# Kernel optimization log

Measured on AMD Instinct MI355X. Metric: run time of the kernel, lower is better.

## Reference

```python
import jax, jax.numpy as jnp
import numpy as np
from jax import lax

NUM_HEADS = 8
EPS = 1e-12  # torch F.normalize default eps


def setup_inputs() -> dict:
    key = jax.random.key(0)
    ks = jax.random.split(key, 7)
    B, C, H, W = 4, 128, 256, 256
    d = C // 2  # per-branch channels = 64
    x = jax.random.normal(ks[0], (B, C, H, W), jnp.float32)
    w_qkv1 = jax.random.normal(ks[1], (3 * d, d), jnp.float32) * 0.05
    w_qkv2 = jax.random.normal(ks[2], (3 * d, d), jnp.float32) * 0.05
    w_dw1 = jax.random.normal(ks[3], (3 * d, 1, 3, 3), jnp.float32) * 0.05
    w_dw2 = jax.random.normal(ks[4], (3 * d, 1, 3, 3), jnp.float32) * 0.05
    w_po1 = jax.random.normal(ks[5], (d, d), jnp.float32) * 0.05
    w_po2 = jax.random.normal(ks[6], (d, d), jnp.float32) * 0.05
    t1 = jnp.ones((NUM_HEADS, 1, 1), jnp.float32)
    t2 = jnp.ones((NUM_HEADS, 1, 1), jnp.float32)
    return {"x": x, "w_qkv1": w_qkv1, "w_qkv2": w_qkv2, "w_dw1": w_dw1,
            "w_dw2": w_dw2, "w_po1": w_po1, "w_po2": w_po2, "t1": t1, "t2": t2}


def _qkv(xb, w1x1, wdw):
    # 1x1 conv (pointwise) then 3x3 depthwise conv, no bias
    y = jnp.einsum('bchw,oc->bohw', xb, w1x1)
    y = lax.conv_general_dilated(
        y, wdw, window_strides=(1, 1), padding='SAME',
        dimension_numbers=('NCHW', 'OIHW', 'NCHW'),
        feature_group_count=y.shape[1])
    return y


def _heads(t, b, h, w):
    # b (head c) h w -> b head c (h*w)
    return t.reshape(b, NUM_HEADS, -1, h * w)


def _l2norm(t):
    n = jnp.sqrt(jnp.sum(t * t, axis=-1, keepdims=True))
    return t / jnp.maximum(n, EPS)


def reference(x, w_qkv1, w_qkv2, w_dw1, w_dw2, w_po1, w_po2, t1, t2):
    b, c, h, w = x.shape
    x1, x2 = jnp.split(x, 2, axis=1)
    q1, k1, v1 = jnp.split(_qkv(x1, w_qkv1, w_dw1), 3, axis=1)
    q2, k2, v2 = jnp.split(_qkv(x2, w_qkv2, w_dw2), 3, axis=1)
    q1, k1, v1 = (_heads(t, b, h, w) for t in (q1, k1, v1))
    q2, k2, v2 = (_heads(t, b, h, w) for t in (q2, k2, v2))
    q1, k1 = _l2norm(q1), _l2norm(k1)
    q2, k2 = _l2norm(q2), _l2norm(k2)
    # channel-wise attention: [b, head, c_h, c_h]
    attn1 = jax.nn.softmax(jnp.einsum('bhcn,bhdn->bhcd', q1, k1) * t1[None], axis=-1)
    attn2 = jax.nn.softmax(jnp.einsum('bhcn,bhdn->bhcd', q2, k2) * t2[None], axis=-1)
    # cross-branch V swap
    out1 = jnp.einsum('bhcd,bhdn->bhcn', attn1, v2).reshape(b, c // 2, h, w)
    out2 = jnp.einsum('bhcd,bhdn->bhcn', attn2, v1).reshape(b, c // 2, h, w)
    out1 = jnp.einsum('bchw,oc->bohw', out1, w_po1)
    out2 = jnp.einsum('bchw,oc->bohw', out2, w_po2)
    return jnp.concatenate([out1, out2], axis=1)
```

## Files before the change

### kernel.cpp

```cpp
#include <hip/hip_runtime.h>
#include <hip/hip_fp16.h>

#define NPIX 65536
#define WIMG 256
#define HIMG 256
#define TW 16
#define TH 8
#define HSTR 24
#define NSLOT 240
#define YCH 248

typedef __attribute__((ext_vector_type(8))) _Float16 half8;
typedef __attribute__((ext_vector_type(4))) float f32x4;

__device__ __forceinline__ unsigned int h2u(__half2 h) {
  union { __half2 h; unsigned int u; } c; c.h = h; return c.u;
}
__device__ __forceinline__ __half2 u2h(unsigned int u) {
  union { unsigned int u; __half2 h; } c; c.u = u; return c.h;
}
__device__ __forceinline__ __half2 sp2(_Float16 s) {
  union { _Float16 h[2]; __half2 v; } u; u.h[0] = s; u.h[1] = s; return u.v;
}
__device__ __forceinline__ int qk_idx(int ch, int pxblk) {
  return ch * 128 + ((pxblk ^ (ch & 7)) << 3);
}
__device__ __forceinline__ void ld16_lds(const void* g, void* l) {
  __builtin_amdgcn_global_load_lds(
      (const __attribute__((address_space(1))) unsigned int*)g,
      (__attribute__((address_space(3))) unsigned int*)l, 16, 0, 0);
}

__global__ __launch_bounds__(256)
void k_prep(const float* __restrict__ wq1, const float* __restrict__ wq2,
            const float* __restrict__ wd1, const float* __restrict__ wd2,
            float* __restrict__ zbuf,
            _Float16* __restrict__ wqh, _Float16* __restrict__ wdh) {
  int i = blockIdx.x * 256 + threadIdx.x;
  if (i < 6144) {
    zbuf[i] = 0.0f;
  } else {
    int j = i - 6144;
    if (j < 24576) {
      int br = j / 12288, r = j - br * 12288;
      wqh[j] = (_Float16)((br ? wq2 : wq1)[r]);
    } else {
      int k = j - 24576;
      int br = k / 3072, r = k - br * 3072;
      int o = r >> 4, t = r & 15;
      wdh[k] = (t < 9) ? (_Float16)((br ? wd2 : wd1)[o * 9 + t]) : (_Float16)0.0f;
    }
  }
}

__global__ __launch_bounds__(256)
void k_xt(const float* __restrict__ x, __half* __restrict__ xT) {
  __shared__ _Float16 tile[64 * 257];
  const int strip = blockIdx.x;
  const int br = blockIdx.y, b = blockIdx.z;
  const int tid = threadIdx.x;
  const float* xb = x + ((size_t)b * 128 + br * 64) * NPIX + strip * 256;
  #pragma unroll 8
  for (int c = 0; c < 64; ++c)
    tile[c * 257 + tid] = (_Float16)xb[(size_t)c * NPIX + tid];
  __syncthreads();
  __half* xo = xT + ((size_t)(b * 2 + br) * NPIX + strip * 256) * 64;
  const int j = tid & 7;
  #pragma unroll
  for (int i = 0; i < 8; ++i) {
    int p = (tid >> 3) + i * 32;
    half8 h;
    #pragma unroll
    for (int k = 0; k < 8; ++k) h[k] = tile[(j * 8 + k) * 257 + p];
    *(half8*)((_Float16*)xo + p * 64 + j * 8) = h;
  }
}

__global__ __launch_bounds__(256, 4)
void k_qkv(const __half* __restrict__ xT,
           const _Float16* __restrict__ wqh, const _Float16* __restrict__ wdh,
           const float* __restrict__ zpage,
           __half* __restrict__ vbuf, float* __restrict__ gram,
           float* __restrict__ sqq, float* __restrict__ sqk)
{
  __shared__ __align__(16) _Float16 xs[256 * 64];
  __shared__ __align__(16) _Float16 ys[16 * YCH];

  const int tid = threadIdx.x;
  const int lane = tid & 63;
  const int wid = tid >> 6;
  const int tile = blockIdx.x;
  const int br = blockIdx.y;
  const int b = blockIdx.z;
  const int tx0 = (tile & 15) * TW;
  const int ty0 = (tile >> 4) * TH;

  const _Float16* wqb = wqh + br * 12288;
  const _Float16* wdb = wdh + br * 3072;
  const __half* xTimg = xT + (size_t)(b * 2 + br) * NPIX * 64;

  {
    const int j = lane & 7, pl = lane >> 3;
    for (int it = wid; it < 30; it += 4) {
      int s = it * 8;
      int slot = s + pl;
      int hy = slot / HSTR;
      int hx = slot - hy * HSTR;
      int gy = ty0 - 1 + hy, gx = tx0 - 1 + hx;
      bool valid = (hx < 18) && ((unsigned)gy < HIMG) && ((unsigned)gx < WIMG);
      const void* src = valid
        ? (const void*)((const _Float16*)xTimg + (size_t)(gy * WIMG + gx) * 64
                        + ((j ^ (slot & 7)) << 3))
        : (const void*)((const char*)zpage + lane * 16);
      ld16_lds(src, (void*)(xs + s * 64));
    }
  }
  asm volatile("s_waitcnt vmcnt(0)" ::: "memory");
  __syncthreads();

  const int col = lane & 15;
  const int qrow = lane >> 4;
  const int rel = wid * 4 + (lane >> 4);
  const int row = (lane >> 1) & 7;
  const int half = lane & 1;

  unsigned int qreg[4][4], kreg[4][4];

#define PW16(P_, G_) do {                                                     \
    const _Float16* wp_ = wqb + ((((P_) * 64 + (G_) * 16 + col) << 6) + qrow * 8); \
    half8 wf0_ = *(const half8*)(wp_);                                        \
    half8 wf1_ = *(const half8*)(wp_ + 32);                                   \
    for (int mt = wid; mt < 15; mt += 4) {                                    \
      int px = mt * 16 + col;                                                 \
      half8 af0 = *(const half8*)(xs + px * 64 + (((qrow    ) ^ (px & 7)) << 3)); \
      half8 af1 = *(const half8*)(xs + px * 64 + (((4 + qrow) ^ (px & 7)) << 3)); \
      f32x4 a0 = {0,0,0,0};                                                   \
      a0 = __builtin_amdgcn_mfma_f32_16x16x32_f16(af0, wf0_, a0, 0, 0, 0);    \
      a0 = __builtin_amdgcn_mfma_f32_16x16x32_f16(af1, wf1_, a0, 0, 0, 0);    \
      int pxd = mt * 16 + qrow * 4;                                           \
      uint2 s0_ = {h2u(__floats2half2_rn(a0[0], a0[1])),                      \
                   h2u(__floats2half2_rn(a0[2], a0[3]))};                     \
      *(uint2*)(ys + col * YCH + pxd) = s0_;                                  \
    }                                                                         \
  } while (0)

#define DW16(P_, G_) do {                                                     \
    const int o_ = (G_) * 16 + rel;                                           \
    const _Float16* wdp_ = wdb + (((P_) * 64 + o_) << 4);                     \
    half8 wv_ = *(const half8*)wdp_;                                          \
    _Float16 w8_ = wdp_[8];                                                   \
    __half2 w2_[9];                                                           \
    _Pragma("unroll")                                                         \
    for (int j = 0; j < 8; ++j) w2_[j] = sp2(wv_[j]);                         \
    w2_[8] = sp2(w8_);                                                        \
    __half2 a_[4];                                                            \
    _Pragma("unroll")                                                         \
    for (int k2 = 0; k2 < 4; ++k2) a_[k2] = u2h(0u);                          \
    _Pragma("unroll")                                                         \
    for (int ky = 0; ky < 3; ++ky) {                                          \
      const _Float16* rp_ = ys + rel * YCH + (row + ky) * HSTR + half * 8;    \
      uint2 ra_ = *(const uint2*)rp_;                                         \
      uint2 rb_ = *(const uint2*)(rp_ + 4);                                   \
      unsigned int rc_ = *(const unsigned int*)(rp_ + 8);                     \
      unsigned int W_[5] = {ra_.x, ra_.y, rb_.x, rb_.y, rc_};                 \
      _Pragma("unroll")                                                       \
      for (int k2 = 0; k2 < 4; ++k2) {                                        \
        unsigned int M_ = (W_[k2] >> 16) | (W_[k2 + 1] << 16);                \
        a_[k2] = __hfma2(w2_[ky * 3 + 0], u2h(W_[k2]), a_[k2]);               \
        a_[k2] = __hfma2(w2_[ky * 3 + 1], u2h(M_), a_[k2]);                   \
        a_[k2] = __hfma2(w2_[ky * 3 + 2], u2h(W_[k2 + 1]), a_[k2]);           \
      }                                                                       \
    }                                                                         \
    if ((P_) == 0) {                                                          \
      _Pragma("unroll")                                                       \
      for (int k2 = 0; k2 < 4; ++k2) qreg[G_][k2] = h2u(a_[k2]);              \
    } else if ((P_) == 1) {                                                   \
      _Pragma("unroll")                                                       \
      for (int k2 = 0; k2 < 4; ++k2) kreg[G_][k2] = h2u(a_[k2]);              \
    } else {                                                                  \
      __half* vrow_ = (__half*)(vbuf                                          \
          + ((size_t)((br * 4 + b) * 64 + o_)) * NPIX                         \
          + (ty0 + row) * WIMG + tx0 + half * 8);                             \
      uint4 s_ = {h2u(a_[0]), h2u(a_[1]), h2u(a_[2]), h2u(a_[3])};            \
      *(uint4*)vrow_ = s_;                                                    \
    }                                                                         \
  } while (0)

  PW16(0, 0); __syncthreads(); DW16(0, 0); __syncthreads();
  PW16(0, 1); __syncthreads(); DW16(0, 1); __syncthreads();
  PW16(0, 2); __syncthreads(); DW16(0, 2); __syncthreads();
  PW16(0, 3); __syncthreads(); DW16(0, 3); __syncthreads();
  PW16(1, 0); __syncthreads(); DW16(1, 0); __syncthreads();
  PW16(1, 1); __syncthreads(); DW16(1, 1); __syncthreads();
  PW16(1, 2); __syncthreads(); DW16(1, 2); __syncthreads();
  PW16(1, 3); __syncthreads(); DW16(1, 3); __syncthreads();
  PW16(2, 0); __syncthreads(); DW16(2, 0); __syncthreads();
  PW16(2, 1); __syncthreads(); DW16(2, 1); __syncthreads();
  PW16(2, 2); __syncthreads(); DW16(2, 2); __syncthreads();
  PW16(2, 3); __syncthreads(); DW16(2, 3);

  {
    _Float16* qsb = xs;
    _Float16* ksb = xs + 64 * 128;
    const int pb = row * 2 + half;
    #pragma unroll
    for (int g = 0; g < 4; ++g) {
      int ch = g * 16 + rel;
      uint4 q_ = {qreg[g][0], qreg[g][1], qreg[g][2], qreg[g][3]};
      uint4 k_ = {kreg[g][0], kreg[g][1], kreg[g][2], kreg[g][3]};
      *(uint4*)(qsb + qk_idx(ch, pb)) = q_;
      *(uint4*)(ksb + qk_idx(ch, pb)) = k_;
    }
  }
  __syncthreads();

  {
    const _Float16* qsb = xs;
    const _Float16* ksb = xs + 64 * 128;
    f32x4 gqk = {0,0,0,0}, gqq = {0,0,0,0}, gkk = {0,0,0,0};
    int ch = wid * 16 + col;
    #pragma unroll
    for (int kc = 0; kc < 4; ++kc) {
      int pb = kc * 4 + qrow;
      half8 aq = *(const half8*)(qsb + qk_idx(ch, pb));
      half8 bk = *(const half8*)(ksb + qk_idx(ch, pb));
      gqk = __builtin_amdgcn_mfma_f32_16x16x32_f16(aq, bk, gqk, 0, 0, 0);
      gqq = __builtin_amdgcn_mfma_f32_16x16x32_f16(aq, aq, gqq, 0, 0, 0);
      gkk = __builtin_amdgcn_mfma_f32_16x16x32_f16(bk, bk, gkk, 0, 0, 0);
    }
    const int gb_off = (br * 4 + b);
    if (((lane >> 3) & 1) == (lane >> 5)) {
      float* gb = gram + gb_off * 512;
      int kch = ch;
      int qc0 = wid * 16 + qrow * 4;
      #pragma unroll
      for (int r = 0; r < 4; ++r) {
        int qch = qc0 + r;
        atomicAdd(&gb[(qch >> 3) * 64 + (qch & 7) * 8 + (kch & 7)], gqk[r]);
      }
    }
    if ((col >> 2) == qrow) {
      atomicAdd(&sqq[gb_off * 64 + ch], gqq[lane & 3]);
      atomicAdd(&sqk[gb_off * 64 + ch], gkk[lane & 3]);
    }
  }
#undef PW16
#undef DW16
}

__global__ __launch_bounds__(64)
void k_attn(const float* __restrict__ gram, const float* __restrict__ sqq,
            const float* __restrict__ sqk,
            const float* __restrict__ wpo1, const float* __restrict__ wpo2,
            const float* __restrict__ t1, const float* __restrict__ t2,
            _Float16* __restrict__ wefft)
{
  const int br = blockIdx.x, b = blockIdx.y;
  const int t = threadIdx.x;
  __shared__ float attn[8][8][8];
  const float* gb = gram + (br * 4 + b) * 512;
  const float* sq = sqq + (br * 4 + b) * 64;
  const float* sk = sqk + (br * 4 + b) * 64;
  const float* tt = br ? t2 : t1;
  {
    int h = t >> 3, cq = t & 7;
    float ts = tt[h];
    float qn = fmaxf(sqrtf(sq[h * 8 + cq]), 1e-12f);
    float lg[8], m = -1e30f;
    #pragma unroll
    for (int d2 = 0; d2 < 8; ++d2) {
      float kn = fmaxf(sqrtf(sk[h * 8 + d2]), 1e-12f);
      lg[d2] = ts * gb[h * 64 + cq * 8 + d2] / (qn * kn);
      m = fmaxf(m, lg[d2]);
    }
    float s = 0.f;
    #pragma unroll
    for (int d2 = 0; d2 < 8; ++d2) { lg[d2] = expf(lg[d2] - m); s += lg[d2]; }
    float inv = 1.0f / s;
    #pragma unroll
    for (int d2 = 0; d2 < 8; ++d2) attn[h][cq][d2] = lg[d2] * inv;
  }
  __syncthreads();
  const float* wpo = br ? wpo2 : wpo1;
  _Float16* wt = wefft + (br * 4 + b) * 4096;
  for (int cp = 0; cp < 64; ++cp) {
    int hp = cp >> 3, ip = cp & 7;
    float acc = 0.f;
    #pragma unroll
    for (int j = 0; j < 8; ++j)
      acc += wpo[t * 64 + hp * 8 + j] * attn[hp][j][ip];
    wt[t * 64 + cp] = (_Float16)acc;
  }
}

__global__ __launch_bounds__(256)
void k_out(const __half* __restrict__ vbuf, const _Float16* __restrict__ wefft,
           float* __restrict__ out)
{
  __shared__ __align__(16) _Float16 vs[64 * 128];
  __shared__ __align__(16) _Float16 vt[128 * 64];

  const int strip = blockIdx.x;
  const int obr = blockIdx.y, b = blockIdx.z;
  const int brv = 1 - obr;
  const int tid = threadIdx.x;
  const int lane = tid & 63;
  const int wid = tid >> 6;
  const int col = lane & 15;
  const int qrow = lane >> 4;

  const __half* vb = vbuf + ((size_t)(brv * 4 + b) * 64) * NPIX + strip * 128;

  for (int i = 0; i < 4; ++i) {
    int it = wid * 4 + i;
    const void* src = (const void*)((const _Float16*)vb
        + (size_t)(it * 4 + (lane >> 4)) * NPIX + (lane & 15) * 8);
    ld16_lds(src, (void*)(vs + it * 512));
  }
  asm volatile("s_waitcnt vmcnt(0)" ::: "memory");
  __syncthreads();

  {
    int px = tid & 127, cb = tid >> 7;
    #pragma unroll
    for (int j = 0; j < 4; ++j) {
      half8 h;
      #pragma unroll
      for (int e = 0; e < 8; ++e) h[e] = vs[(cb * 32 + j * 8 + e) * 128 + px];
      int chunk = cb * 4 + j;
      *(half8*)(vt + ((px * 8 + (chunk ^ (px & 7))) << 3)) = h;
    }
  }
  __syncthreads();

  const _Float16* wt = wefft + (obr * 4 + b) * 4096;
  half8 bf[2][4];
  #pragma unroll
  for (int nt = 0; nt < 4; ++nt)
    #pragma unroll
    for (int kc = 0; kc < 2; ++kc)
      bf[kc][nt] = *(const half8*)(wt + (nt * 16 + col) * 64 + kc * 32 + qrow * 8);

  float* ob = out + ((size_t)b * 128 + obr * 64) * NPIX + strip * 128;
  #pragma unroll
  for (int mi = 0; mi < 2; ++mi) {
    int mt = wid * 2 + mi;
    int px = mt * 16 + col;
    half8 af0 = *(const half8*)(vt + ((px * 8 + ((qrow    ) ^ (px & 7))) << 3));
    half8 af1 = *(const half8*)(vt + ((px * 8 + ((4 + qrow) ^ (px & 7))) << 3));
    f32x4 acc[4] = {{0,0,0,0},{0,0,0,0},{0,0,0,0},{0,0,0,0}};
    #pragma unroll
    for (int nt = 0; nt < 4; ++nt) {
      acc[nt] = __builtin_amdgcn_mfma_f32_16x16x32_f16(af0, bf[0][nt], acc[nt], 0, 0, 0);
      acc[nt] = __builtin_amdgcn_mfma_f32_16x16x32_f16(af1, bf[1][nt], acc[nt], 0, 0, 0);
    }
    int pxd = mt * 16 + qrow * 4;
    #pragma unroll
    for (int nt = 0; nt < 4; ++nt) {
      float4 s = {acc[nt][0], acc[nt][1], acc[nt][2], acc[nt][3]};
      *(float4*)(ob + (size_t)(nt * 16 + col) * NPIX + pxd) = s;
    }
  }
}

extern "C" void kernel_launch(void* const* d_in, const int* in_sizes, int n_in,
                              void* d_out, int out_size, void* d_ws, size_t ws_size,
                              hipStream_t stream) {
  const float* x     = (const float*)d_in[0];
  const float* wqkv1 = (const float*)d_in[1];
  const float* wqkv2 = (const float*)d_in[2];
  const float* wdw1  = (const float*)d_in[3];
  const float* wdw2  = (const float*)d_in[4];
  const float* wpo1  = (const float*)d_in[5];
  const float* wpo2  = (const float*)d_in[6];
  const float* t1    = (const float*)d_in[7];
  const float* t2    = (const float*)d_in[8];

  char* ws = (char*)d_ws;
  __half* vbuf = (__half*)ws;
  float* gram  = (float*)(ws + 67108864);
  float* sqq   = gram + 4096;
  float* sqk   = sqq + 512;
  float* zpage = sqk + 512;
  _Float16* wqkvh = (_Float16*)(zpage + 1024);
  _Float16* wdwh  = wqkvh + 24576;
  _Float16* wefft = wdwh + 6144;

  __half* xT = (__half*)d_out;

  k_prep<<<dim3(144), dim3(256), 0, stream>>>(wqkv1, wqkv2, wdw1, wdw2,
                                              gram, wqkvh, wdwh);
  k_xt<<<dim3(256, 2, 4), dim3(256), 0, stream>>>(x, xT);
  k_qkv<<<dim3(512, 2, 4), dim3(256), 0, stream>>>(xT, wqkvh, wdwh,
                                                   zpage, vbuf, gram, sqq, sqk);
  k_attn<<<dim3(2, 4), dim3(64), 0, stream>>>(gram, sqq, sqk, wpo1, wpo2, t1, t2, wefft);
  k_out<<<dim3(512, 2, 4), dim3(256), 0, stream>>>(vbuf, wefft, (float*)d_out);
}
```

Before: 240.9 us.

## Process 32 channels per pointwise/depthwise phase with prefetched weights

The fused qkv kernel now handles 32 output channels per phase instead of 16. That halves the number of pointwise/depthwise phases and their barriers, and each thread's depthwise pass covers a full 16-pixel row. Weights for the next phase are loaded into registers ahead of time (double buffering), and the q/k scatter to shared memory moves inside the final phase. The ys buffer doubles and launch bounds drop to 3 blocks per SM, so occupancy may fall in exchange for fewer syncs and wider per-thread work.

```diff
diff --git a/kernel.cpp b/kernel.cpp
--- a/kernel.cpp
+++ b/kernel.cpp
@@ -76,7 +76,7 @@
   }
 }
 
-__global__ __launch_bounds__(256, 4)
+__global__ __launch_bounds__(256, 3)
 void k_qkv(const __half* __restrict__ xT,
            const _Float16* __restrict__ wqh, const _Float16* __restrict__ wdh,
            const float* __restrict__ zpage,
@@ -84,7 +84,7 @@
            float* __restrict__ sqq, float* __restrict__ sqk)
 {
   __shared__ __align__(16) _Float16 xs[256 * 64];
-  __shared__ __align__(16) _Float16 ys[16 * YCH];
+  __shared__ __align__(16) _Float16 ys[32 * YCH];
 
   const int tid = threadIdx.x;
   const int lane = tid & 63;
@@ -120,99 +120,117 @@
 
   const int col = lane & 15;
   const int qrow = lane >> 4;
-  const int rel = wid * 4 + (lane >> 4);
-  const int row = (lane >> 1) & 7;
-  const int half = lane & 1;
-
-  unsigned int qreg[4][4], kreg[4][4];
-
-#define PW16(P_, G_) do {                                                     \
-    const _Float16* wp_ = wqb + ((((P_) * 64 + (G_) * 16 + col) << 6) + qrow * 8); \
-    half8 wf0_ = *(const half8*)(wp_);                                        \
-    half8 wf1_ = *(const half8*)(wp_ + 32);                                   \
+  const int oo = tid >> 3;
+  const int row = tid & 7;
+
+  unsigned int qreg[2][8], kreg[2][8];
+
+#define LOADW(P_, H_, F00, F01, F10, F11, WV, W8) do {                        \
+    const _Float16* wp_ = wqb + ((((P_) * 64 + (H_) * 32 + col) << 6) + qrow * 8); \
+    F00 = *(const half8*)(wp_);                                               \
+    F10 = *(const half8*)(wp_ + 32);                                          \
+    F01 = *(const half8*)(wp_ + 1024);                                        \
+    F11 = *(const half8*)(wp_ + 1024 + 32);                                   \
+    const _Float16* wdp_ = wdb + ((((P_) * 64 + (H_) * 32 + oo)) << 4);       \
+    WV = *(const half8*)wdp_;                                                 \
+    W8 = wdp_[8];                                                             \
+} while (0)
+
+#define PHASE(P_, H_, F00, F01, F10, F11, WV, W8) do {                        \
     for (int mt = wid; mt < 15; mt += 4) {                                    \
       int px = mt * 16 + col;                                                 \
       half8 af0 = *(const half8*)(xs + px * 64 + (((qrow    ) ^ (px & 7)) << 3)); \
       half8 af1 = *(const half8*)(xs + px * 64 + (((4 + qrow) ^ (px & 7)) << 3)); \
-      f32x4 a0 = {0,0,0,0};                                                   \
-      a0 = __builtin_amdgcn_mfma_f32_16x16x32_f16(af0, wf0_, a0, 0, 0, 0);    \
-      a0 = __builtin_amdgcn_mfma_f32_16x16x32_f16(af1, wf1_, a0, 0, 0, 0);    \
+      f32x4 a0 = {0,0,0,0}, a1 = {0,0,0,0};                                   \
+      a0 = __builtin_amdgcn_mfma_f32_16x16x32_f16(af0, F00, a0, 0, 0, 0);     \
+      a0 = __builtin_amdgcn_mfma_f32_16x16x32_f16(af1, F10, a0, 0, 0, 0);     \
+      a1 = __builtin_amdgcn_mfma_f32_16x16x32_f16(af0, F01, a1, 0, 0, 0);     \
+      a1 = __builtin_amdgcn_mfma_f32_16x16x32_f16(af1, F11, a1, 0, 0, 0);     \
       int pxd = mt * 16 + qrow * 4;                                           \
-      uint2 s0_ = {h2u(__floats2half2_rn(a0[0], a0[1])),                      \
-                   h2u(__floats2half2_rn(a0[2], a0[3]))};                     \
-      *(uint2*)(ys + col * YCH + pxd) = s0_;                                  \
+      __half2* d0 = (__half2*)(ys + (col     ) * YCH + pxd);                  \
+      __half2* d1 = (__half2*)(ys + (col + 16) * YCH + pxd);                  \
+      d0[0] = __floats2half2_rn(a0[0], a0[1]);                                \
+      d0[1] = __floats2half2_rn(a0[2], a0[3]);                                \
+      d1[0] = __floats2half2_rn(a1[0], a1[1]);                                \
+      d1[1] = __floats2half2_rn(a1[2], a1[3]);                                \
     }                                                                         \
-  } while (0)
-
-#define DW16(P_, G_) do {                                                     \
-    const int o_ = (G_) * 16 + rel;                                           \
-    const _Float16* wdp_ = wdb + (((P_) * 64 + o_) << 4);                     \
-    half8 wv_ = *(const half8*)wdp_;                                          \
-    _Float16 w8_ = wdp_[8];                                                   \
-    __half2 w2_[9];                                                           \
-    _Pragma("unroll")                                                         \
-    for (int j = 0; j < 8; ++j) w2_[j] = sp2(wv_[j]);                         \
-    w2_[8] = sp2(w8_);                                                        \
-    __half2 a_[4];                                                            \
-    _Pragma("unroll")                                                         \
-    for (int k2 = 0; k2 < 4; ++k2) a_[k2] = u2h(0u);                          \
-    _Pragma("unroll")                                                         \
-    for (int ky = 0; ky < 3; ++ky) {                                          \
-      const _Float16* rp_ = ys + rel * YCH + (row + ky) * HSTR + half * 8;    \
-      uint2 ra_ = *(const uint2*)rp_;                                         \
-      uint2 rb_ = *(const uint2*)(rp_ + 4);                                   \
-      unsigned int rc_ = *(const unsigned int*)(rp_ + 8);                     \
-      unsigned int W_[5] = {ra_.x, ra_.y, rb_.x, rb_.y, rc_};                 \
+    __syncthreads();                                                          \
+    {                                                                         \
+      const int o_ = (H_) * 32 + oo;                                          \
+      __half2 w2_[9];                                                         \
       _Pragma("unroll")                                                       \
-      for (int k2 = 0; k2 < 4; ++k2) {                                        \
-        unsigned int M_ = (W_[k2] >> 16) | (W_[k2 + 1] << 16);                \
-        a_[k2] = __hfma2(w2_[ky * 3 + 0], u2h(W_[k2]), a_[k2]);               \
-        a_[k2] = __hfma2(w2_[ky * 3 + 1], u2h(M_), a_[k2]);                   \
-        a_[k2] = __hfma2(w2_[ky * 3 + 2], u2h(W_[k2 + 1]), a_[k2]);           \
+      for (int j = 0; j < 8; ++j) w2_[j] = sp2(WV[j]);                        \
+      w2_[8] = sp2(W8);                                                       \
+      __half2 a_[8];                                                          \
+      _Pragma("unroll")                                                       \
+      for (int k2 = 0; k2 < 8; ++k2) a_[k2] = u2h(0u);                        \
+      _Pragma("unroll")                                                       \
+      for (int ky = 0; ky < 3; ++ky) {                                        \
+        const _Float16* rp_ = ys + oo * YCH + (row + ky) * HSTR;              \
+        uint4 ra_ = *(const uint4*)rp_;                                       \
+        uint4 rb_ = *(const uint4*)(rp_ + 8);                                 \
+        unsigned int rc_ = *(const unsigned int*)(rp_ + 16);                  \
+        unsigned int A_[9] = {ra_.x, ra_.y, ra_.z, ra_.w,                     \
+                              rb_.x, rb_.y, rb_.z, rb_.w, rc_};               \
+        _Pragma("unroll")                                                     \
+        for (int k2 = 0; k2 < 8; ++k2) {                                      \
+          unsigned int M_ = (A_[k2] >> 16) | (A_[k2 + 1] << 16);              \
+          a_[k2] = __hfma2(w2_[ky * 3 + 0], u2h(A_[k2]), a_[k2]);             \
+          a_[k2] = __hfma2(w2_[ky * 3 + 1], u2h(M_), a_[k2]);                 \
+          a_[k2] = __hfma2(w2_[ky * 3 + 2], u2h(A_[k2 + 1]), a_[k2]);         \
+        }                                                                     \
+      }                                                                       \
+      if ((P_) == 0) {                                                        \
+        _Pragma("unroll")                                                     \
+        for (int k2 = 0; k2 < 8; ++k2) qreg[H_][k2] = h2u(a_[k2]);            \
+      } else if ((P_) == 1) {                                                 \
+        _Pragma("unroll")                                                     \
+        for (int k2 = 0; k2 < 8; ++k2) kreg[H_][k2] = h2u(a_[k2]);            \
+      } else {                                                                \
+        __half* vrow_ = (__half*)(vbuf                                        \
+            + ((size_t)((br * 4 + b) * 64 + o_)) * NPIX                       \
+            + (ty0 + row) * WIMG + tx0);                                      \
+        uint4 s0_ = {h2u(a_[0]), h2u(a_[1]), h2u(a_[2]), h2u(a_[3])};         \
+        uint4 s1_ = {h2u(a_[4]), h2u(a_[5]), h2u(a_[6]), h2u(a_[7])};         \
+        *(uint4*)vrow_ = s0_;                                                 \
+        *(uint4*)(vrow_ + 8) = s1_;                                           \
+        if ((H_) == 1) {                                                      \
+          _Float16* qsb_ = xs;                                                \
+          _Float16* ksb_ = xs + 64 * 128;                                     \
+          _Pragma("unroll")                                                   \
+          for (int hh = 0; hh < 2; ++hh) {                                    \
+            int ch = hh * 32 + oo;                                            \
+            uint4 q0_ = {qreg[hh][0], qreg[hh][1], qreg[hh][2], qreg[hh][3]}; \
+            uint4 q1_ = {qreg[hh][4], qreg[hh][5], qreg[hh][6], qreg[hh][7]}; \
+            uint4 k0_ = {kreg[hh][0], kreg[hh][1], kreg[hh][2], kreg[hh][3]}; \
+            uint4 k1_ = {kreg[hh][4], kreg[hh][5], kreg[hh][6], kreg[hh][7]}; \
+            *(uint4*)(qsb_ + qk_idx(ch, 2 * row))     = q0_;                  \
+            *(uint4*)(qsb_ + qk_idx(ch, 2 * row + 1)) = q1_;                  \
+            *(uint4*)(ksb_ + qk_idx(ch, 2 * row))     = k0_;                  \
+            *(uint4*)(ksb_ + qk_idx(ch, 2 * row + 1)) = k1_;                  \
+          }                                                                   \
+        }                                                                     \
       }                                                                       \
     }                                                                         \
-    if ((P_) == 0) {                                                          \
-      _Pragma("unroll")                                                       \
-      for (int k2 = 0; k2 < 4; ++k2) qreg[G_][k2] = h2u(a_[k2]);              \
-    } else if ((P_) == 1) {                                                   \
-      _Pragma("unroll")                                                       \
-      for (int k2 = 0; k2 < 4; ++k2) kreg[G_][k2] = h2u(a_[k2]);              \
-    } else {                                                                  \
-      __half* vrow_ = (__half*)(vbuf                                          \
-          + ((size_t)((br * 4 + b) * 64 + o_)) * NPIX                         \
-          + (ty0 + row) * WIMG + tx0 + half * 8);                             \
-      uint4 s_ = {h2u(a_[0]), h2u(a_[1]), h2u(a_[2]), h2u(a_[3])};            \
-      *(uint4*)vrow_ = s_;                                                    \
-    }                                                                         \
-  } while (0)
-
-  PW16(0, 0); __syncthreads(); DW16(0, 0); __syncthreads();
-  PW16(0, 1); __syncthreads(); DW16(0, 1); __syncthreads();
-  PW16(0, 2); __syncthreads(); DW16(0, 2); __syncthreads();
-  PW16(0, 3); __syncthreads(); DW16(0, 3); __syncthreads();
-  PW16(1, 0); __syncthreads(); DW16(1, 0); __syncthreads();
-  PW16(1, 1); __syncthreads(); DW16(1, 1); __syncthreads();
-  PW16(1, 2); __syncthreads(); DW16(1, 2); __syncthreads();
-  PW16(1, 3); __syncthreads(); DW16(1, 3); __syncthreads();
-  PW16(2, 0); __syncthreads(); DW16(2, 0); __syncthreads();
-  PW16(2, 1); __syncthreads(); DW16(2, 1); __syncthreads();
-  PW16(2, 2); __syncthreads(); DW16(2, 2); __syncthreads();
-  PW16(2, 3); __syncthreads(); DW16(2, 3);
-
-  {
-    _Float16* qsb = xs;
-    _Float16* ksb = xs + 64 * 128;
-    const int pb = row * 2 + half;
-    #pragma unroll
-    for (int g = 0; g < 4; ++g) {
-      int ch = g * 16 + rel;
-      uint4 q_ = {qreg[g][0], qreg[g][1], qreg[g][2], qreg[g][3]};
-      uint4 k_ = {kreg[g][0], kreg[g][1], kreg[g][2], kreg[g][3]};
-      *(uint4*)(qsb + qk_idx(ch, pb)) = q_;
-      *(uint4*)(ksb + qk_idx(ch, pb)) = k_;
-    }
-  }
-  __syncthreads();
+    __syncthreads();                                                          \
+} while (0)
+
+  half8 Af00, Af01, Af10, Af11, Awv;
+  half8 Bf00, Bf01, Bf10, Bf11, Bwv;
+  _Float16 Aw8, Bw8;
+
+  LOADW(0, 0, Af00, Af01, Af10, Af11, Awv, Aw8);
+  LOADW(0, 1, Bf00, Bf01, Bf10, Bf11, Bwv, Bw8);
+  PHASE(0, 0, Af00, Af01, Af10, Af11, Awv, Aw8);
+  LOADW(1, 0, Af00, Af01, Af10, Af11, Awv, Aw8);
+  PHASE(0, 1, Bf00, Bf01, Bf10, Bf11, Bwv, Bw8);
+  LOADW(1, 1, Bf00, Bf01, Bf10, Bf11, Bwv, Bw8);
+  PHASE(1, 0, Af00, Af01, Af10, Af11, Awv, Aw8);
+  LOADW(2, 0, Af00, Af01, Af10, Af11, Awv, Aw8);
+  PHASE(1, 1, Bf00, Bf01, Bf10, Bf11, Bwv, Bw8);
+  LOADW(2, 1, Bf00, Bf01, Bf10, Bf11, Bwv, Bw8);
+  PHASE(2, 0, Af00, Af01, Af10, Af11, Awv, Aw8);
+  PHASE(2, 1, Bf00, Bf01, Bf10, Bf11, Bwv, Bw8);
 
   {
     const _Float16* qsb = xs;
@@ -244,8 +262,8 @@
       atomicAdd(&sqk[gb_off * 64 + ch], gkk[lane & 3]);
     }
   }
-#undef PW16
-#undef DW16
+#undef LOADW
+#undef PHASE
 }
 
 __global__ __launch_bounds__(64)
```

After: 220.8 us. 8.3% less time.
